# Kernel optimization log

Measured on AMD Instinct MI355X. Metric: run time of the kernel, lower is better.

Reference implementation:

```python
import jax, jax.numpy as jnp
import numpy as np

B, T, H, NH = 4, 1024, 1024, 16
HS = H // NH
FF = 4 * H
EPS = 1e-5


def setup_inputs() -> dict:
    key = jax.random.key(0)
    ks = jax.random.split(key, 12)
    s = 0.02
    inp = {
        "x": jax.random.normal(ks[0], (B, T, H), jnp.float32),
        # attention projections, stored as [in, out] so y = x @ W + b
        "Wq": jax.random.normal(ks[1], (H, H), jnp.float32) * s,
        "bq": jnp.zeros((H,), jnp.float32),
        "Wk": jax.random.normal(ks[2], (H, H), jnp.float32) * s,
        "bk": jnp.zeros((H,), jnp.float32),
        "Wv": jax.random.normal(ks[3], (H, H), jnp.float32) * s,
        "bv": jnp.zeros((H,), jnp.float32),
        "Wo": jax.random.normal(ks[4], (H, H), jnp.float32) * s,
        "bo": jnp.zeros((H,), jnp.float32),
        # layernorms
        "ln1_w": jnp.ones((H,), jnp.float32),
        "ln1_b": jnp.zeros((H,), jnp.float32),
        "ln2_w": jnp.ones((H,), jnp.float32),
        "ln2_b": jnp.zeros((H,), jnp.float32),
        # MLP
        "Wfc": jax.random.normal(ks[5], (H, FF), jnp.float32) * s,
        "bfc": jnp.zeros((FF,), jnp.float32),
        "Wpr": jax.random.normal(ks[6], (FF, H), jnp.float32) * s,
        "bpr": jnp.zeros((H,), jnp.float32),
    }
    return inp


def _layernorm(x, w, b):
    mu = jnp.mean(x, axis=-1, keepdims=True)
    var = jnp.mean(jnp.square(x - mu), axis=-1, keepdims=True)
    return (x - mu) * jax.lax.rsqrt(var + EPS) * w + b


def _rope(x):
    # x: [B, nh, T, hs]; interleaved-pair RoPE, base 10000
    half = HS // 2
    inv_freq = 1.0 / (10000.0 ** (jnp.arange(half, dtype=jnp.float32) / half))
    ang = jnp.arange(T, dtype=jnp.float32)[:, None] * inv_freq[None, :]  # [T, half]
    cos, sin = jnp.cos(ang), jnp.sin(ang)
    xr = x.reshape(*x.shape[:-1], half, 2)
    x0, x1 = xr[..., 0], xr[..., 1]
    r0 = x0 * cos - x1 * sin
    r1 = x0 * sin + x1 * cos
    return jnp.stack([r0, r1], axis=-1).reshape(x.shape)


def _block(x, Wq, bq, Wk, bk, Wv, bv, Wo, bo, ln1_w, ln1_b, ln2_w, ln2_b, Wfc, bfc, Wpr, bpr):
    # --- attention sub-block ---
    h1 = _layernorm(x, ln1_w, ln1_b)
    q = (h1 @ Wq + bq).reshape(B, T, NH, HS).transpose(0, 2, 1, 3)  # [B,nh,T,hs]
    k = (h1 @ Wk + bk).reshape(B, T, NH, HS).transpose(0, 2, 1, 3)
    v = (h1 @ Wv + bv).reshape(B, T, NH, HS).transpose(0, 2, 1, 3)
    q, k = _rope(q), _rope(k)
    scores = jnp.einsum('bhqd,bhkd->bhqk', q, k) / jnp.sqrt(jnp.float32(HS))
    attn = jax.nn.softmax(scores, axis=-1)
    # NOTE: original applies the causal mask AFTER softmax (multiplicative, no renorm)
    causal = jnp.tril(jnp.ones((T, T), jnp.float32))[None, None]
    attn = attn * causal
    out = jnp.einsum('bhqk,bhkd->bhqd', attn, v)
    out = out.transpose(0, 2, 1, 3).reshape(B, T, H)
    x = x + (out @ Wo + bo)
    # --- MLP sub-block ---
    h2 = _layernorm(x, ln2_w, ln2_b)
    m = jax.nn.gelu(h2 @ Wfc + bfc, approximate=False)
    x = x + (m @ Wpr + bpr)
    return x


def reference(x, Wq, bq, Wk, bk, Wv, bv, Wo, bo, ln1_w, ln1_b, ln2_w, ln2_b, Wfc, bfc, Wpr, bpr):
    return _block(x, Wq, bq, Wk, bk, Wv, bv, Wo, bo, ln1_w, ln1_b, ln2_w, ln2_b, Wfc, bfc, Wpr, bpr)
```

## Files before the change

### kernel.cpp

```cpp
#include <hip/hip_runtime.h>
#include <hip/hip_bf16.h>

typedef unsigned short u16;
typedef __attribute__((ext_vector_type(8))) short bf16x8;
typedef __attribute__((ext_vector_type(4))) float f32x4;
typedef __attribute__((ext_vector_type(4))) unsigned short u16x4;

#define B_  4
#define T_  1024
#define H_  1024
#define NH_ 16
#define HS_ 64
#define FF_ 4096
#define M_  (B_*T_)
#define QKV_S 3072

__device__ __forceinline__ u16 f2bf(float f){
  union { float f; unsigned u; } v; v.f = f;
  unsigned r = v.u + 0x7fffu + ((v.u >> 16) & 1u);
  return (u16)(r >> 16);
}
__device__ __forceinline__ float bf2f(u16 h){
  union { unsigned u; float f; } v; v.u = ((unsigned)h) << 16;
  return v.f;
}
__device__ __forceinline__ unsigned pack2bf(float a, float b){
  __hip_bfloat162 h = __float22bfloat162_rn(make_float2(a, b));
  union { __hip_bfloat162 h; unsigned u; } c; c.h = h;
  return c.u;
}

__device__ __forceinline__ void gload_lds16(const void* g, void* l){
  __builtin_amdgcn_global_load_lds(
      (const __attribute__((address_space(1))) unsigned int*)g,
      (__attribute__((address_space(3))) unsigned int*)l,
      16, 0, 0);
}

__device__ __forceinline__ void trans_tile(const float* __restrict__ W,
                                           u16* __restrict__ Wt, int K, int N,
                                           int k0, int n0, int tid)
{
  __shared__ u16 tile[64][68];
  #pragma unroll
  for (int it = 0; it < 4; ++it){
    int ci = tid + it * 256;
    int kr = ci >> 4, nc = ci & 15;
    float4 f = *(const float4*)(W + (size_t)(k0 + kr) * N + n0 + nc * 4);
    tile[kr][nc*4+0] = f2bf(f.x);
    tile[kr][nc*4+1] = f2bf(f.y);
    tile[kr][nc*4+2] = f2bf(f.z);
    tile[kr][nc*4+3] = f2bf(f.w);
  }
  __syncthreads();
  #pragma unroll
  for (int it = 0; it < 4; ++it){
    int co = tid + it * 256;
    int nr = co >> 4, kc = co & 15;
    u16x4 o;
    o[0] = tile[kc*4+0][nr];
    o[1] = tile[kc*4+1][nr];
    o[2] = tile[kc*4+2][nr];
    o[3] = tile[kc*4+3][nr];
    *(u16x4*)(Wt + (size_t)(n0 + nr) * K + k0 + kc * 4) = o;
  }
}

__global__ __launch_bounds__(256) void trans_qkvo_k(
    const float* __restrict__ Wq, const float* __restrict__ Wk,
    const float* __restrict__ Wv, const float* __restrict__ Wo,
    u16* __restrict__ WqkvT, u16* __restrict__ WoT)
{
  const int z = blockIdx.z;
  const float* src = (z == 0) ? Wq : (z == 1) ? Wk : (z == 2) ? Wv : Wo;
  u16* dst = (z == 3) ? WoT : (WqkvT + (size_t)z * 1024 * 1024);
  trans_tile(src, dst, H_, H_, blockIdx.y * 64, blockIdx.x * 64, threadIdx.x);
}

__global__ __launch_bounds__(256) void transpose_cvt(const float* __restrict__ W,
                                                     u16* __restrict__ Wt, int K, int N)
{
  trans_tile(W, Wt, K, N, blockIdx.y * 64, blockIdx.x * 64, threadIdx.x);
}

__global__ __launch_bounds__(256) void vtrans_k(const u16* __restrict__ qkv,
                                                u16* __restrict__ vtg)
{
  __shared__ u16 tile[64][72];
  const int bh = blockIdx.y, tt = blockIdx.x * 64;
  const int b = bh >> 4, h = bh & 15;
  const size_t src = (size_t)b * T_ * QKV_S + h * HS_ + 2048;
  const int tid = threadIdx.x;
  #pragma unroll
  for (int it = 0; it < 2; ++it){
    int ci = tid + it * 256;
    int r = ci >> 3, c = ci & 7;
    bf16x8 vvv = *(const bf16x8*)(qkv + src + (size_t)(tt + r) * QKV_S + c * 8);
    *(bf16x8*)&tile[r][c * 8] = vvv;
  }
  __syncthreads();
  #pragma unroll
  for (int it = 0; it < 2; ++it){
    int co = tid + it * 256;
    int d = co >> 3, c = co & 7;
    bf16x8 ov;
    #pragma unroll
    for (int j = 0; j < 8; ++j) ov[j] = (short)tile[c * 8 + j][d];
    *(bf16x8*)(vtg + (size_t)bh * HS_ * T_ + (size_t)d * T_ + tt + c * 8) = ov;
  }
}

__global__ void prep_small_k(const float* __restrict__ a, const float* __restrict__ b,
                             const float* __restrict__ c, float* __restrict__ o,
                             float* __restrict__ tab){
  int i = blockIdx.x * 256 + threadIdx.x;
  if (i < QKV_S){
    o[i] = (i < 1024) ? a[i] : (i < 2048) ? b[i - 1024] : c[i - 2048];
  } else {
    int j = i - QKV_S;
    if (j < T_ * 32){
      int t = j >> 5, f = j & 31;
      float inv = powf(10000.0f, -(float)f * (1.0f / 32.0f));
      float ang = (float)t * inv;
      tab[j*2+0] = cosf(ang);
      tab[j*2+1] = sinf(ang);
    }
  }
}

__global__ __launch_bounds__(256) void ln_kernel(const float* __restrict__ x,
    const float* __restrict__ w, const float* __restrict__ bgain,
    u16* __restrict__ out)
{
  const int row = blockIdx.x;
  const int t = threadIdx.x;
  float4 vv = ((const float4*)(x + (size_t)row * H_))[t];
  float s  = vv.x + vv.y + vv.z + vv.w;
  float s2 = vv.x*vv.x + vv.y*vv.y + vv.z*vv.z + vv.w*vv.w;
  #pragma unroll
  for (int mm = 1; mm < 64; mm <<= 1){ s += __shfl_xor(s, mm); s2 += __shfl_xor(s2, mm); }
  __shared__ float red[8];
  int wid = t >> 6;
  if ((t & 63) == 0){ red[wid] = s; red[4 + wid] = s2; }
  __syncthreads();
  s  = red[0] + red[1] + red[2] + red[3];
  s2 = red[4] + red[5] + red[6] + red[7];
  float mu  = s * (1.0f / H_);
  float var = s2 * (1.0f / H_) - mu * mu;
  float rin = rsqrtf(var + 1e-5f);
  float4 wv = ((const float4*)w)[t];
  float4 bv = ((const float4*)bgain)[t];
  u16x4 ov;
  ov[0] = f2bf((vv.x - mu) * rin * wv.x + bv.x);
  ov[1] = f2bf((vv.y - mu) * rin * wv.y + bv.y);
  ov[2] = f2bf((vv.z - mu) * rin * wv.z + bv.z);
  ov[3] = f2bf((vv.w - mu) * rin * wv.w + bv.w);
  ((u16x4*)(out + (size_t)row * H_))[t] = ov;
}

template<int EPI>
__global__ __launch_bounds__(512, 1) void gemm8p_kernel(
    const u16* __restrict__ A, const u16* __restrict__ Bt,
    const float* __restrict__ bias, const float* __restrict__ rtab,
    void* __restrict__ Cout, int M, int N, int K)
{
  __shared__ __attribute__((aligned(16))) u16 Abuf[2][2][8192];
  __shared__ __attribute__((aligned(16))) u16 Bbuf[2][2][8192];
  const int tid  = threadIdx.x;
  const int lane = tid & 63;
  const int wid  = tid >> 6;
  const int wm = wid >> 2, wn = wid & 3;
  const int lrow = lane & 15, lkg = lane >> 4;

  const int gx  = gridDim.x;
  const int nwg = gx * gridDim.y;
  const int wg  = blockIdx.y * gx + blockIdx.x;
  const int nx  = nwg >> 3;
  const int swz = (wg & 7) * nx + (wg >> 3);
  const int m0 = (swz / gx) * 256, n0 = (swz % gx) * 256;

  const int r0 = tid >> 2, c0 = tid & 3;
  const int sc = c0 ^ ((r0 >> 1) & 3);
  const u16* As0 = A  + (size_t)(m0 + r0) * K + sc * 8;
  const u16* As1 = As0 + (size_t)128 * K;
  const u16* Bs0 = Bt + (size_t)(n0 + r0) * K + sc * 8;
  const u16* Bs1 = Bs0 + (size_t)128 * K;
  const int dlo = tid * 8, dhi = (tid + 512) * 8;

  int aoff[8], boff[4];
  #pragma unroll
  for (int mi = 0; mi < 8; ++mi){
    int r = wm*128 + mi*16 + lrow;
    aoff[mi] = (r*4 + (lkg ^ ((r >> 1) & 3))) * 16;
  }
  #pragma unroll
  for (int ni = 0; ni < 4; ++ni){
    int r = wn*64 + ni*16 + lrow;
    boff[ni] = (r*4 + (lkg ^ ((r >> 1) & 3))) * 16;
  }

  f32x4 acc[8][4] = {};
  const int NT = K >> 6;

  gload_lds16(As0,      &Abuf[0][0][dlo]); gload_lds16(As1,      &Abuf[0][0][dhi]);
  gload_lds16(Bs0,      &Bbuf[0][0][dlo]); gload_lds16(Bs1,      &Bbuf[0][0][dhi]);
  gload_lds16(As0 + 32, &Abuf[0][1][dlo]); gload_lds16(As1 + 32, &Abuf[0][1][dhi]);
  gload_lds16(Bs0 + 32, &Bbuf[0][1][dlo]); gload_lds16(Bs1 + 32, &Bbuf[0][1][dhi]);
  asm volatile("s_waitcnt vmcnt(4)" ::: "memory");
  __builtin_amdgcn_s_barrier();

  for (int t = 0; t < NT; ++t){
    const int cb = t & 1, nb = (t + 1) & 1;
    const int koff = (t + 1) << 6;
    const char* Ak0 = (const char*)&Abuf[cb][0][0];
    const char* Ak1 = (const char*)&Abuf[cb][1][0];
    const char* Bk0 = (const char*)&Bbuf[cb][0][0];
    const char* Bk1 = (const char*)&Bbuf[cb][1][0];
    const bool pre = (t + 1 < NT);
    bf16x8 af[8], bf[4];

    #pragma unroll
    for (int mi = 0; mi < 8; ++mi) af[mi] = *(const bf16x8*)(Ak0 + aoff[mi]);
    bf[0] = *(const bf16x8*)(Bk0 + boff[0]);
    bf[1] = *(const bf16x8*)(Bk0 + boff[1]);
    if (pre){ gload_lds16(As0 + koff, &Abuf[nb][0][dlo]);
              gload_lds16(As1 + koff, &Abuf[nb][0][dhi]); }
    __builtin_amdgcn_s_barrier();
    asm volatile("s_waitcnt lgkmcnt(0)" ::: "memory");
    __builtin_amdgcn_sched_barrier(0);
    __builtin_amdgcn_s_setprio(1);
    #pragma unroll
    for (int mi = 0; mi < 8; ++mi){
      acc[mi][0] = __builtin_amdgcn_mfma_f32_16x16x32_bf16(bf[0], af[mi], acc[mi][0], 0, 0, 0);
      acc[mi][1] = __builtin_amdgcn_mfma_f32_16x16x32_bf16(bf[1], af[mi], acc[mi][1], 0, 0, 0);
    }
    __builtin_amdgcn_s_setprio(0);
    __builtin_amdgcn_s_barrier();

    bf[2] = *(const bf16x8*)(Bk0 + boff[2]);
    bf[3] = *(const bf16x8*)(Bk0 + boff[3]);
    if (pre){ gload_lds16(Bs0 + koff, &Bbuf[nb][0][dlo]);
              gload_lds16(Bs1 + koff, &Bbuf[nb][0][dhi]); }
    __builtin_amdgcn_s_barrier();
    asm volatile("s_waitcnt lgkmcnt(0)" ::: "memory");
    __builtin_amdgcn_sched_barrier(0);
    __builtin_amdgcn_s_setprio(1);
    #pragma unroll
    for (int mi = 0; mi < 8; ++mi){
      acc[mi][2] = __builtin_amdgcn_mfma_f32_16x16x32_bf16(bf[2], af[mi], acc[mi][2], 0, 0, 0);
      acc[mi][3] = __builtin_amdgcn_mfma_f32_16x16x32_bf16(bf[3], af[mi], acc[mi][3], 0, 0, 0);
    }
    __builtin_amdgcn_s_setprio(0);
    if (pre) asm volatile("s_waitcnt vmcnt(4)" ::: "memory");
    else     asm volatile("s_waitcnt vmcnt(0)" ::: "memory");
    __builtin_amdgcn_s_barrier();

    #pragma unroll
    for (int mi = 0; mi < 8; ++mi) af[mi] = *(const bf16x8*)(Ak1 + aoff[mi]);
    bf[0] = *(const bf16x8*)(Bk1 + boff[0]);
    bf[1] = *(const bf16x8*)(Bk1 + boff[1]);
    if (pre){ gload_lds16(As0 + koff + 32, &Abuf[nb][1][dlo]);
              gload_lds16(As1 + koff + 32, &Abuf[nb][1][dhi]); }
    __builtin_amdgcn_s_barrier();
    asm volatile("s_waitcnt lgkmcnt(0)" ::: "memory");
    __builtin_amdgcn_sched_barrier(0);
    __builtin_amdgcn_s_setprio(1);
    #pragma unroll
    for (int mi = 0; mi < 8; ++mi){
      acc[mi][0] = __builtin_amdgcn_mfma_f32_16x16x32_bf16(bf[0], af[mi], acc[mi][0], 0, 0, 0);
      acc[mi][1] = __builtin_amdgcn_mfma_f32_16x16x32_bf16(bf[1], af[mi], acc[mi][1], 0, 0, 0);
    }
    __builtin_amdgcn_s_setprio(0);
    __builtin_amdgcn_s_barrier();

    bf[2] = *(const bf16x8*)(Bk1 + boff[2]);
    bf[3] = *(const bf16x8*)(Bk1 + boff[3]);
    if (pre){ gload_lds16(Bs0 + koff + 32, &Bbuf[nb][1][dlo]);
              gload_lds16(Bs1 + koff + 32, &Bbuf[nb][1][dhi]); }
    __builtin_amdgcn_s_barrier();
    asm volatile("s_waitcnt lgkmcnt(0)" ::: "memory");
    __builtin_amdgcn_sched_barrier(0);
    __builtin_amdgcn_s_setprio(1);
    #pragma unroll
    for (int mi = 0; mi < 8; ++mi){
      acc[mi][2] = __builtin_amdgcn_mfma_f32_16x16x32_bf16(bf[2], af[mi], acc[mi][2], 0, 0, 0);
      acc[mi][3] = __builtin_amdgcn_mfma_f32_16x16x32_bf16(bf[3], af[mi], acc[mi][3], 0, 0, 0);
    }
    __builtin_amdgcn_s_setprio(0);
    if (pre) asm volatile("s_waitcnt vmcnt(4)" ::: "memory");
    __builtin_amdgcn_s_barrier();
  }

  #pragma unroll
  for (int mi = 0; mi < 8; ++mi){
    int row = m0 + wm*128 + mi*16 + lrow;
    #pragma unroll
    for (int ni = 0; ni < 4; ++ni){
      int col0 = n0 + wn*64 + ni*16 + lkg*4;
      float4 bv = *(const float4*)(bias + col0);
      float v0 = acc[mi][ni][0] + bv.x;
      float v1 = acc[mi][ni][1] + bv.y;
      float v2 = acc[mi][ni][2] + bv.z;
      float v3 = acc[mi][ni][3] + bv.w;
      if (EPI == 1){
        float u0 = 0.7978845608f * v0 + 0.0356774081f * v0 * v0 * v0;
        float u1 = 0.7978845608f * v1 + 0.0356774081f * v1 * v1 * v1;
        float u2 = 0.7978845608f * v2 + 0.0356774081f * v2 * v2 * v2;
        float u3 = 0.7978845608f * v3 + 0.0356774081f * v3 * v3 * v3;
        float e0 = exp2f(u0 * 2.8853900818f);
        float e1 = exp2f(u1 * 2.8853900818f);
        float e2 = exp2f(u2 * 2.8853900818f);
        float e3 = exp2f(u3 * 2.8853900818f);
        v0 = v0 - v0 / (e0 + 1.0f);
        v1 = v1 - v1 / (e1 + 1.0f);
        v2 = v2 - v2 / (e2 + 1.0f);
        v3 = v3 - v3 / (e3 + 1.0f);
      }
      if (EPI == 2){
        if (col0 < 2048){
          int tt = row & (T_ - 1);
          const float* rt = rtab + ((size_t)tt * 32 + ((col0 & 63) >> 1)) * 2;
          float cc0 = rt[0], ss0 = rt[1], cc1 = rt[2], ss1 = rt[3];
          float q0 = v0 * cc0 - v1 * ss0, q1 = v0 * ss0 + v1 * cc0;
          float q2 = v2 * cc1 - v3 * ss1, q3 = v2 * ss1 + v3 * cc1;
          if (col0 < 1024){
            const float qs = 0.125f * 1.44269504f;
            q0 *= qs; q1 *= qs; q2 *= qs; q3 *= qs;
          }
          v0 = q0; v1 = q1; v2 = q2; v3 = q3;
        }
      }
      uint2 ov;
      ov.x = pack2bf(v0, v1);
      ov.y = pack2bf(v2, v3);
      *(uint2*)((u16*)Cout + (size_t)row * N + col0) = ov;
    }
  }
}

__global__ __launch_bounds__(256, 2) void gemm64_kernel(
    const u16* __restrict__ A, const u16* __restrict__ Bt,
    const float* __restrict__ bias, const float* __restrict__ res,
    float* __restrict__ Cout, int M, int N, int K)
{
  __shared__ __attribute__((aligned(16))) u16 As[3][64 * 64];
  __shared__ __attribute__((aligned(16))) u16 Bs[3][128 * 64];
  const int tid  = threadIdx.x;
  const int lane = tid & 63;
  const int wid  = tid >> 6;
  const int wm = wid >> 1, wn = wid & 1;
  const int lrow = lane & 15, lkg = lane >> 4;

  const int gx  = gridDim.x;
  const int nwg = gx * gridDim.y;
  const int wg  = blockIdx.y * gx + blockIdx.x;
  const int nx  = nwg >> 3;
  const int swz = (wg & 7) * nx + (wg >> 3);
  const int m0 = (swz / gx) * 64, n0 = (swz % gx) * 128;

  const int sr = tid >> 3;
  const int sc8 = tid & 7;
  const int scs = (sc8 & 4) | ((sc8 & 3) ^ ((sr >> 1) & 3));
  const u16* Asrc0 = A + (size_t)(m0 + sr) * K + scs * 8;
  const u16* Asrc1 = Asrc0 + (size_t)32 * K;
  const u16* Bsrc0 = Bt + (size_t)(n0 + sr) * K + scs * 8;
  const u16* Bsrc1 = Bsrc0 + (size_t)32 * K;
  const u16* Bsrc2 = Bsrc0 + (size_t)64 * K;
  const u16* Bsrc3 = Bsrc0 + (size_t)96 * K;
  const int dA0 = tid * 8,        dA1 = (tid + 256) * 8;
  const int dB0 = tid * 8,        dB1 = (tid + 256) * 8;
  const int dB2 = (tid + 512) * 8, dB3 = (tid + 768) * 8;

  int aoff[2][2], boff[4][2];
  #pragma unroll
  for (int kh = 0; kh < 2; ++kh){
    #pragma unroll
    for (int mi = 0; mi < 2; ++mi){
      int r = wm*32 + mi*16 + lrow;
      aoff[mi][kh] = (r*8 + kh*4 + (lkg ^ ((r >> 1) & 3))) * 16;
    }
    #pragma unroll
    for (int ni = 0; ni < 4; ++ni){
      int r = wn*64 + ni*16 + lrow;
      boff[ni][kh] = (r*8 + kh*4 + (lkg ^ ((r >> 1) & 3))) * 16;
    }
  }

  f32x4 acc[2][4] = {};
  const int NT = K >> 6;

  #pragma unroll
  for (int s = 0; s < 2; ++s){
    int k0 = s << 6;
    gload_lds16(Asrc0 + k0, &As[s][dA0]);
    gload_lds16(Asrc1 + k0, &As[s][dA1]);
    gload_lds16(Bsrc0 + k0, &Bs[s][dB0]);
    gload_lds16(Bsrc1 + k0, &Bs[s][dB1]);
    gload_lds16(Bsrc2 + k0, &Bs[s][dB2]);
    gload_lds16(Bsrc3 + k0, &Bs[s][dB3]);
  }

  int rs = 0, wsl = 2;
  for (int t = 0; t < NT; ++t){
    if (t < NT - 1) asm volatile("s_waitcnt vmcnt(6)" ::: "memory");
    else            asm volatile("s_waitcnt vmcnt(0)" ::: "memory");
    __builtin_amdgcn_s_barrier();

    const char* Ab = (const char*)&As[rs][0];
    const char* Bb = (const char*)&Bs[rs][0];
    rs = (rs + 1 == 3) ? 0 : rs + 1;

    bf16x8 af[2][2], bfr[4][2];
    #pragma unroll
    for (int kh = 0; kh < 2; ++kh){
      #pragma unroll
      for (int mi = 0; mi < 2; ++mi)
        af[mi][kh] = *(const bf16x8*)(Ab + aoff[mi][kh]);
      #pragma unroll
      for (int ni = 0; ni < 4; ++ni)
        bfr[ni][kh] = *(const bf16x8*)(Bb + boff[ni][kh]);
    }
    __builtin_amdgcn_sched_barrier(0);

    if (t + 2 < NT){
      int k0 = (t + 2) << 6;
      gload_lds16(Asrc0 + k0, &As[wsl][dA0]);
      gload_lds16(Asrc1 + k0, &As[wsl][dA1]);
      gload_lds16(Bsrc0 + k0, &Bs[wsl][dB0]);
      gload_lds16(Bsrc1 + k0, &Bs[wsl][dB1]);
      gload_lds16(Bsrc2 + k0, &Bs[wsl][dB2]);
      gload_lds16(Bsrc3 + k0, &Bs[wsl][dB3]);
    }
    wsl = (wsl + 1 == 3) ? 0 : wsl + 1;

    #pragma unroll
    for (int kh = 0; kh < 2; ++kh)
      #pragma unroll
      for (int mi = 0; mi < 2; ++mi)
        #pragma unroll
        for (int ni = 0; ni < 4; ++ni)
          acc[mi][ni] = __builtin_amdgcn_mfma_f32_16x16x32_bf16(
              bfr[ni][kh], af[mi][kh], acc[mi][ni], 0, 0, 0);
  }

  #pragma unroll
  for (int mi = 0; mi < 2; ++mi){
    int row = m0 + wm*32 + mi*16 + lrow;
    #pragma unroll
    for (int ni = 0; ni < 4; ++ni){
      int col0 = n0 + wn*64 + ni*16 + lkg*4;
      float4 bv = *(const float4*)(bias + col0);
      float4 rv = *(const float4*)(res + (size_t)row * N + col0);
      float4 ov;
      ov.x = acc[mi][ni][0] + bv.x + rv.x;
      ov.y = acc[mi][ni][1] + bv.y + rv.y;
      ov.z = acc[mi][ni][2] + bv.z + rv.z;
      ov.w = acc[mi][ni][3] + bv.w + rv.w;
      *(float4*)(Cout + (size_t)row * N + col0) = ov;
    }
  }
}

__global__ __launch_bounds__(512, 4) void attn_kernel(
    const u16* __restrict__ qkv, const u16* __restrict__ vtg,
    u16* __restrict__ out)
{
  __shared__ u16 K_lds[3][64 * 64];
  __shared__ u16 VT_lds[3][64 * 64];
  __shared__ u16 P_lds[8][16 * 64];
  const int tid = threadIdx.x, lane = tid & 63, w = tid >> 6;
  const int lrow = lane & 15, lkg = lane >> 4;
  const int q0 = blockIdx.x * 128;
  const int bh = blockIdx.y, b = bh >> 4, h = bh & 15;
  const size_t baseq  = (size_t)b * T_ * QKV_S + h * HS_;
  const size_t basek  = baseq + 1024;
  const size_t basevt = (size_t)bh * HS_ * T_;
  const size_t baseo  = (size_t)b * T_ * H_ + h * HS_;
  const int qg = q0 + w * 16 + lrow;

  bf16x8 qa[2];
  {
    const u16* qp = qkv + baseq + (size_t)qg * QKV_S + lkg * 8;
    qa[0] = *(const bf16x8*)qp;
    qa[1] = *(const bf16x8*)(qp + 32);
  }

  const int r0 = tid >> 3, c0 = tid & 7, g0 = c0 ^ (r0 & 7);
  const u16* kap = qkv + basek + (size_t)r0 * QKV_S + g0 * 8;
  const u16* vap = vtg + basevt + (size_t)r0 * T_ + g0 * 8;
  const int kd = tid * 8;

  f32x4 o[4] = {};
  float mrun = -1e30f, lrun = 0.f;

  #pragma unroll
  for (int s = 0; s < 2; ++s){
    gload_lds16(kap + (size_t)s * 64 * QKV_S, &K_lds[s][kd]);
    gload_lds16(vap + s * 64,                 &VT_lds[s][kd]);
  }

  int rs = 0, wsl = 2;
  for (int t = 0; t < 16; ++t){
    const int kt = t << 6;
    if (t < 15) asm volatile("s_waitcnt vmcnt(2)" ::: "memory");
    else        asm volatile("s_waitcnt vmcnt(0)" ::: "memory");
    __builtin_amdgcn_s_barrier();
    __builtin_amdgcn_sched_barrier(0);

    if (t + 2 < 16){
      gload_lds16(kap + (size_t)(t + 2) * 64 * QKV_S, &K_lds[wsl][kd]);
      gload_lds16(vap + (t + 2) * 64,                 &VT_lds[wsl][kd]);
    }
    wsl = (wsl + 1 == 3) ? 0 : wsl + 1;

    const u16* Kc  = K_lds[rs];
    const u16* VTc = VT_lds[rs];
    rs = (rs + 1 == 3) ? 0 : rs + 1;

    f32x4 s[4];
    __builtin_amdgcn_s_setprio(1);
    #pragma unroll
    for (int mi = 0; mi < 4; ++mi){
      f32x4 c = {};
      #pragma unroll
      for (int ss = 0; ss < 2; ++ss){
        int r = mi * 16 + lrow;
        int off = r * 128 + (((ss * 4 + lkg) ^ (r & 7)) * 16);
        bf16x8 kb = *(const bf16x8*)((const char*)Kc + off);
        c = __builtin_amdgcn_mfma_f32_16x16x32_bf16(kb, qa[ss], c, 0, 0, 0);
      }
      s[mi] = c;
    }
    __builtin_amdgcn_s_setprio(0);

    float mt = fmaxf(fmaxf(fmaxf(s[0][0], s[0][1]), fmaxf(s[0][2], s[0][3])),
                     fmaxf(fmaxf(s[1][0], s[1][1]), fmaxf(s[1][2], s[1][3])));
    mt = fmaxf(mt, fmaxf(fmaxf(fmaxf(s[2][0], s[2][1]), fmaxf(s[2][2], s[2][3])),
                         fmaxf(fmaxf(s[3][0], s[3][1]), fmaxf(s[3][2], s[3][3]))));
    mt = fmaxf(mt, __shfl_xor(mt, 16));
    mt = fmaxf(mt, __shfl_xor(mt, 32));
    if (!__all(mt <= mrun + 8.f)){
      float mnew = fmaxf(mrun, mt);
      float fsc = exp2f(mrun - mnew);
      lrun *= fsc;
      #pragma unroll
      for (int nf = 0; nf < 4; ++nf){
        #pragma unroll
        for (int r = 0; r < 4; ++r) o[nf][r] *= fsc;
      }
      mrun = mnew;
    }

    float p[16];
    float ls = 0.f;
    #pragma unroll
    for (int mi = 0; mi < 4; ++mi){
      #pragma unroll
      for (int r = 0; r < 4; ++r){
        int key = kt + mi * 16 + lkg * 4 + r;
        float pv = exp2f(s[mi][r] - mrun);
        ls += pv;
        p[mi * 4 + r] = (key <= qg) ? pv : 0.f;
      }
    }
    ls += __shfl_xor(ls, 16);
    ls += __shfl_xor(ls, 32);
    lrun += ls;

    if (kt <= q0 + w * 16 + 15){
      char* pbase = (char*)&P_lds[w][0];
      const int rx = (lrow & 7) << 4;
      #pragma unroll
      for (int mi = 0; mi < 4; ++mi){
        uint2 pk;
        pk.x = pack2bf(p[mi*4+0], p[mi*4+1]);
        pk.y = pack2bf(p[mi*4+2], p[mi*4+3]);
        *(uint2*)(pbase + (lrow * 128 + ((mi * 32 + lkg * 8) ^ rx))) = pk;
      }
      __builtin_amdgcn_s_setprio(1);
      #pragma unroll
      for (int ss = 0; ss < 2; ++ss){
        bf16x8 pb = *(const bf16x8*)(pbase + (lrow * 128 + ((ss * 64 + lkg * 16) ^ rx)));
        #pragma unroll
        for (int nfd = 0; nfd < 4; ++nfd){
          int d = nfd * 16 + lrow;
          int off = d * 128 + (((ss * 4 + lkg) ^ (d & 7)) * 16);
          bf16x8 vb = *(const bf16x8*)((const char*)VTc + off);
          o[nfd] = __builtin_amdgcn_mfma_f32_16x16x32_bf16(vb, pb, o[nfd], 0, 0, 0);
        }
      }
      __builtin_amdgcn_s_setprio(0);
    }
  }

  float rl = 1.0f / lrun;
  #pragma unroll
  for (int nfd = 0; nfd < 4; ++nfd){
    uint2 ov;
    ov.x = pack2bf(o[nfd][0] * rl, o[nfd][1] * rl);
    ov.y = pack2bf(o[nfd][2] * rl, o[nfd][3] * rl);
    *(uint2*)(out + baseo + (size_t)qg * H_ + nfd * 16 + lkg * 4) = ov;
  }
}

extern "C" void kernel_launch(void* const* d_in, const int* in_sizes, int n_in,
                              void* d_out, int out_size, void* d_ws, size_t ws_size,
                              hipStream_t stream)
{
  (void)in_sizes; (void)n_in; (void)out_size; (void)ws_size;
  const float* x    = (const float*)d_in[0];
  const float* Wq   = (const float*)d_in[1];
  const float* bq   = (const float*)d_in[2];
  const float* Wk   = (const float*)d_in[3];
  const float* bk   = (const float*)d_in[4];
  const float* Wv   = (const float*)d_in[5];
  const float* bv   = (const float*)d_in[6];
  const float* Wo   = (const float*)d_in[7];
  const float* bo   = (const float*)d_in[8];
  const float* ln1w = (const float*)d_in[9];
  const float* ln1b = (const float*)d_in[10];
  const float* ln2w = (const float*)d_in[11];
  const float* ln2b = (const float*)d_in[12];
  const float* Wfc  = (const float*)d_in[13];
  const float* bfc  = (const float*)d_in[14];
  const float* Wpr  = (const float*)d_in[15];
  const float* bpr  = (const float*)d_in[16];

  char* ws = (char*)d_ws;
  u16*  WqkvT = (u16*)(ws + ((size_t) 0 << 20));
  u16*  WoT   = (u16*)(ws + ((size_t) 6 << 20));
  u16*  WfcT  = (u16*)(ws + ((size_t) 8 << 20));
  u16*  WprT  = (u16*)(ws + ((size_t)16 << 20));
  u16*  h1    = (u16*)(ws + ((size_t)24 << 20));
  u16*  qkvb  = (u16*)(ws + ((size_t)32 << 20));
  float* x1   = (float*)(ws + ((size_t)32 << 20));
  u16*  h2    = (u16*)(ws + ((size_t)48 << 20));
  float* bqkv = (float*)(ws + ((size_t)56 << 20));
  float* rtab = (float*)(ws + ((size_t)56 << 20) + (64 << 10));
  u16*  vtg   = (u16*)(ws + ((size_t)57 << 20));
  u16*  mb    = (u16*)(ws + ((size_t)56 << 20));
  u16*  attnout = h1;

  dim3 blk(256);
  dim3 gblk(512);

  trans_qkvo_k<<<dim3(H_/64, H_/64, 4), blk, 0, stream>>>(Wq, Wk, Wv, Wo, WqkvT, WoT);
  transpose_cvt<<<dim3(FF_/64, H_/64),  blk, 0, stream>>>(Wfc, WfcT, H_,  FF_);
  transpose_cvt<<<dim3(H_/64,  FF_/64), blk, 0, stream>>>(Wpr, WprT, FF_, H_);
  prep_small_k<<<dim3((QKV_S + T_*32 + 255)/256), blk, 0, stream>>>(bq, bk, bv, bqkv, rtab);

  ln_kernel<<<dim3(M_), blk, 0, stream>>>(x, ln1w, ln1b, h1);
  gemm8p_kernel<2><<<dim3(QKV_S/256, M_/256), gblk, 0, stream>>>(h1, WqkvT, bqkv, rtab, qkvb, M_, QKV_S, H_);
  vtrans_k<<<dim3(T_/64, B_*NH_), blk, 0, stream>>>(qkvb, vtg);
  attn_kernel<<<dim3(T_/128, B_*NH_), dim3(512), 0, stream>>>(qkvb, vtg, attnout);
  gemm64_kernel<<<dim3(H_/128, M_/64), blk, 0, stream>>>(attnout, WoT, bo, x, x1, M_, H_, H_);
  ln_kernel<<<dim3(M_), blk, 0, stream>>>(x1, ln2w, ln2b, h2);
  gemm8p_kernel<1><<<dim3(FF_/256, M_/256), gblk, 0, stream>>>(h2, WfcT, bfc, nullptr, mb, M_, FF_, H_);
  gemm64_kernel<<<dim3(H_/128, M_/64), blk, 0, stream>>>(mb, WprT, bpr, x1, (float*)d_out, M_, H_, FF_);
}
```

Measured before the change: 239.1 us.

## Double-buffer attention K/V tiles and raise occupancy bound

Cuts the attention kernel's K/V LDS ring from three stages to two, issuing the next-next tile load after a second barrier at the end of each iteration into the buffer just consumed. Less shared memory lets the launch bound go from 4 to 6 blocks per CU. The row-max reduction is rewritten as three-input max chains and the softmax sum as a tree, with masking split into its own pass. In exchange each iteration gets an extra barrier, loads are issued later so there is less overlap, and the tighter register budget could cause spills.

```diff
diff --git a/kernel.cpp b/kernel.cpp
--- a/kernel.cpp
+++ b/kernel.cpp
@@ -28,6 +28,9 @@
   __hip_bfloat162 h = __float22bfloat162_rn(make_float2(a, b));
   union { __hip_bfloat162 h; unsigned u; } c; c.h = h;
   return c.u;
+}
+__device__ __forceinline__ float max3f(float a, float b, float c){
+  return fmaxf(fmaxf(a, b), c);
 }
 
 __device__ __forceinline__ void gload_lds16(const void* g, void* l){
@@ -461,12 +464,12 @@
   }
 }
 
-__global__ __launch_bounds__(512, 4) void attn_kernel(
+__global__ __launch_bounds__(512, 6) void attn_kernel(
     const u16* __restrict__ qkv, const u16* __restrict__ vtg,
     u16* __restrict__ out)
 {
-  __shared__ u16 K_lds[3][64 * 64];
-  __shared__ u16 VT_lds[3][64 * 64];
+  __shared__ u16 K_lds[2][64 * 64];
+  __shared__ u16 VT_lds[2][64 * 64];
   __shared__ u16 P_lds[8][16 * 64];
   const int tid = threadIdx.x, lane = tid & 63, w = tid >> 6;
   const int lrow = lane & 15, lkg = lane >> 4;
@@ -499,7 +502,7 @@
     gload_lds16(vap + s * 64,                 &VT_lds[s][kd]);
   }
 
-  int rs = 0, wsl = 2;
+  int cur = 0;
   for (int t = 0; t < 16; ++t){
     const int kt = t << 6;
     if (t < 15) asm volatile("s_waitcnt vmcnt(2)" ::: "memory");
@@ -507,15 +510,8 @@
     __builtin_amdgcn_s_barrier();
     __builtin_amdgcn_sched_barrier(0);
 
-    if (t + 2 < 16){
-      gload_lds16(kap + (size_t)(t + 2) * 64 * QKV_S, &K_lds[wsl][kd]);
-      gload_lds16(vap + (t + 2) * 64,                 &VT_lds[wsl][kd]);
-    }
-    wsl = (wsl + 1 == 3) ? 0 : wsl + 1;
-
-    const u16* Kc  = K_lds[rs];
-    const u16* VTc = VT_lds[rs];
-    rs = (rs + 1 == 3) ? 0 : rs + 1;
+    const u16* Kc  = K_lds[cur];
+    const u16* VTc = VT_lds[cur];
 
     f32x4 s[4];
     __builtin_amdgcn_s_setprio(1);
@@ -533,10 +529,12 @@
     }
     __builtin_amdgcn_s_setprio(0);
 
-    float mt = fmaxf(fmaxf(fmaxf(s[0][0], s[0][1]), fmaxf(s[0][2], s[0][3])),
-                     fmaxf(fmaxf(s[1][0], s[1][1]), fmaxf(s[1][2], s[1][3])));
-    mt = fmaxf(mt, fmaxf(fmaxf(fmaxf(s[2][0], s[2][1]), fmaxf(s[2][2], s[2][3])),
-                         fmaxf(fmaxf(s[3][0], s[3][1]), fmaxf(s[3][2], s[3][3]))));
+    float t0 = max3f(s[0][0], s[0][1], s[0][2]);
+    float t1 = max3f(s[0][3], s[1][0], s[1][1]);
+    float t2 = max3f(s[1][2], s[1][3], s[2][0]);
+    float t3 = max3f(s[2][1], s[2][2], s[2][3]);
+    float t4 = max3f(s[3][0], s[3][1], s[3][2]);
+    float mt = fmaxf(max3f(t0, t1, t2), max3f(t3, t4, s[3][3]));
     mt = fmaxf(mt, __shfl_xor(mt, 16));
     mt = fmaxf(mt, __shfl_xor(mt, 32));
     if (!__all(mt <= mrun + 8.f)){
@@ -551,21 +549,31 @@
       mrun = mnew;
     }
 
-    float p[16];
-    float ls = 0.f;
+    float pv[16];
     #pragma unroll
     for (int mi = 0; mi < 4; ++mi){
       #pragma unroll
-      for (int r = 0; r < 4; ++r){
-        int key = kt + mi * 16 + lkg * 4 + r;
-        float pv = exp2f(s[mi][r] - mrun);
-        ls += pv;
-        p[mi * 4 + r] = (key <= qg) ? pv : 0.f;
-      }
-    }
+      for (int r = 0; r < 4; ++r)
+        pv[mi * 4 + r] = exp2f(s[mi][r] - mrun);
+    }
+    float a0 = (pv[0] + pv[1]) + (pv[2] + pv[3]);
+    float a1 = (pv[4] + pv[5]) + (pv[6] + pv[7]);
+    float a2 = (pv[8] + pv[9]) + (pv[10] + pv[11]);
+    float a3 = (pv[12] + pv[13]) + (pv[14] + pv[15]);
+    float ls = (a0 + a1) + (a2 + a3);
     ls += __shfl_xor(ls, 16);
     ls += __shfl_xor(ls, 32);
     lrun += ls;
+
+    float p[16];
+    #pragma unroll
+    for (int mi = 0; mi < 4; ++mi){
+      #pragma unroll
+      for (int r = 0; r < 4; ++r){
+        int key = kt + mi * 16 + lkg * 4 + r;
+        p[mi * 4 + r] = (key <= qg) ? pv[mi * 4 + r] : 0.f;
+      }
+    }
 
     if (kt <= q0 + w * 16 + 15){
       char* pbase = (char*)&P_lds[w][0];
@@ -591,6 +599,13 @@
       }
       __builtin_amdgcn_s_setprio(0);
     }
+
+    __builtin_amdgcn_s_barrier();
+    if (t + 2 < 16){
+      gload_lds16(kap + (size_t)(t + 2) * 64 * QKV_S, &K_lds[cur][kd]);
+      gload_lds16(vap + (t + 2) * 64,                 &VT_lds[cur][kd]);
+    }
+    cur ^= 1;
   }
 
   float rl = 1.0f / lrun;
```

Result: no change. 236.7 us (-1.0%).
